# Kernel tuning notes

Measured on AMD Instinct MI355X. Metric: run time of the kernel, lower is better.

The kernel has to match this reference:

```python
import jax, jax.numpy as jnp
import numpy as np

L = 2048
E = 1024
H = 16
D = E // H


def setup_inputs() -> dict:
    key = jax.random.key(0)
    ks = jax.random.split(key, 9)
    inp = {
        "values": jax.random.normal(ks[0], (L, E), dtype=jnp.float32),
        "keys": jax.random.normal(ks[1], (L, E), dtype=jnp.float32),
        "query": jax.random.normal(ks[2], (L, E), dtype=jnp.float32),
        "dist_matrix": jax.random.uniform(ks[3], (L, L), dtype=jnp.float32),
        "Wv": jax.random.normal(ks[4], (E, E), dtype=jnp.float32) * 0.02,
        "Wk": jax.random.normal(ks[5], (E, E), dtype=jnp.float32) * 0.02,
        "Wq": jax.random.normal(ks[6], (E, E), dtype=jnp.float32) * 0.02,
        "Wo": jax.random.normal(ks[7], (E, E), dtype=jnp.float32) * 0.02,
        "bo": jax.random.normal(ks[8], (E,), dtype=jnp.float32) * 0.02,
    }
    return inp


def reference(values, keys, query, dist_matrix, Wv, Wk, Wq, Wo, bo):
    # Linear projections (torch Linear: x @ W.T), then split heads: [L, H, D]
    v = (values @ Wv.T).reshape(L, H, D)
    k = (keys @ Wk.T).reshape(L, H, D)
    q = (query @ Wq.T).reshape(L, H, D)

    # energy: [H, Lq, Lk]
    energy = jnp.einsum("qhd,khd->hqk", q, k)

    # distance bias: zeros -> inf, then 1/(d+1); broadcast over heads
    dm = jnp.where(dist_matrix == 0, jnp.inf, dist_matrix)
    bias = 1.0 / (dm + 1.0)
    energy = energy + bias[None, :, :]

    attn = jax.nn.softmax(energy / jnp.sqrt(jnp.float32(E)), axis=2)

    out = jnp.einsum("hql,lhd->qhd", attn, v).reshape(L, H * D)
    return out @ Wo.T + bo
```

## Files before the change

### kernel.cpp

```cpp
#include <hip/hip_runtime.h>


#define L_SEQ 2048
#define E_DIM 1024
#define H_HEADS 16
#define D_HEAD 64
#define KSPLIT 4
#define OSPLIT 2

typedef unsigned short u16;
typedef unsigned int u32;
typedef __attribute__((ext_vector_type(8))) short bf16x8;
typedef __attribute__((ext_vector_type(8))) unsigned short u16x8;
typedef __attribute__((ext_vector_type(4))) unsigned short u16x4;
typedef __attribute__((ext_vector_type(4))) float f32x4;

#define C_LOG2E_32 0.045084220027780106f

__device__ __forceinline__ float bf2f(u16 u) {
  union { u32 i; float f; } v; v.i = ((u32)u) << 16; return v.f;
}
__device__ __forceinline__ u16 f2bf(float f) {
  union { float f; u32 i; } v; v.f = f;
  u32 u = v.i;
  u += 0x7FFFu + ((u >> 16) & 1u);
  return (u16)(u >> 16);
}
__device__ __forceinline__ u32 pack_bf16_pair(float lo, float hi) {
  union { float f; u32 u; } a, b;
  a.f = lo; b.f = hi;
  return __builtin_amdgcn_perm(b.u + 0x8000u, a.u + 0x8000u, 0x07060302u);
}
__device__ __forceinline__ void gload16(const u16* g, u16* l) {
  __builtin_amdgcn_global_load_lds(
      (const __attribute__((address_space(1))) u32*)g,
      (__attribute__((address_space(3))) u32*)l, 16, 0, 0);
}

__global__ void cvt_all(const float* __restrict__ xq, const float* __restrict__ xk,
                        const float* __restrict__ xv,
                        const float* __restrict__ wq, const float* __restrict__ wk,
                        const float* __restrict__ wv, const float* __restrict__ wo,
                        const float* __restrict__ dist, const float* __restrict__ bo,
                        u16* oq, u16* ok, u16* ov,
                        u16* owq, u16* owk, u16* owv, u16* owo, u16* obias,
                        float* __restrict__ outp)
{
  size_t gid = (size_t)blockIdx.x * 256 + threadIdx.x;
  const size_t NQ = 524288;
  const size_t NW = 262144;
  const size_t DL = 1048576;
  const size_t FILL = 3 * NQ + 4 * NW + DL;

  if (gid >= FILL) {
    size_t off = (gid - FILL) * 4;
    int n = (int)(off & (E_DIM - 1));
    *(f32x4*)&outp[off] = *(const f32x4*)&bo[n];
    return;
  }

  const float* src; u16* dst; size_t off; bool isb = false;
  if      (gid <     NQ)           { src = xq;   dst = oq;    off = gid; }
  else if (gid < 2 * NQ)           { src = xk;   dst = ok;    off = gid - NQ; }
  else if (gid < 3 * NQ)           { src = xv;   dst = ov;    off = gid - 2 * NQ; }
  else if (gid < 3 * NQ + NW)      { src = wq;   dst = owq;   off = gid - 3 * NQ; }
  else if (gid < 3 * NQ + 2 * NW)  { src = wk;   dst = owk;   off = gid - 3 * NQ - NW; }
  else if (gid < 3 * NQ + 3 * NW)  { src = wv;   dst = owv;   off = gid - 3 * NQ - 2 * NW; }
  else if (gid < 3 * NQ + 4 * NW)  { src = wo;   dst = owo;   off = gid - 3 * NQ - 3 * NW; }
  else { src = dist; dst = obias; off = gid - 3 * NQ - 4 * NW; isb = true; }

  f32x4 v = *(const f32x4*)&src[off * 4];
  u16x4 o;
#pragma unroll
  for (int j = 0; j < 4; ++j) {
    float f = v[j];
    if (isb) f = (f == 0.f) ? 0.f : C_LOG2E_32 / (f + 1.f);
    o[j] = f2bf(f);
  }
  *(u16x4*)&dst[off * 4] = o;
}

#define TM 64
#define TN 128
#define BK 32

template<int OUTMODE>
__global__ __launch_bounds__(256, 4) void gemm_pd(
    const u16* __restrict__ A0, const u16* __restrict__ B0, void* __restrict__ C0,
    const u16* __restrict__ A1, const u16* __restrict__ B1, void* __restrict__ C1,
    const u16* __restrict__ A2, const u16* __restrict__ B2, void* __restrict__ C2,
    int M, int N, int K)
{
  const u16* A; const u16* B; void* C;
  if (OUTMODE == 2)         { A = A0; B = B0; C = C0; }
  else if (blockIdx.z == 0) { A = A0; B = B0; C = C0; }
  else if (blockIdx.z == 1) { A = A1; B = B1; C = C1; }
  else                      { A = A2; B = B2; C = C2; }

  __shared__ __align__(16) u16 As[2][TM * BK];
  __shared__ __align__(16) u16 Bs[2][TN * BK];

  const int m0 = blockIdx.y * TM;
  const int n0 = blockIdx.x * TN;
  const int t = threadIdx.x;
  const int wave = t >> 6;
  const int lane = t & 63;
  const int quad = lane >> 4;
  const int col  = lane & 15;
  const int wm = (wave >> 1) * 32;
  const int wn = (wave & 1) * 64;

  const int sr = lane >> 2;
  const int sg = ((lane & 3) ^ ((lane >> 3) & 3)) * 8;
  const u16* gA  = A + (size_t)(m0 + wave * 16 + sr) * K + sg;
  const u16* gB0 = B + (size_t)(n0 + wave * 16 + sr) * K + sg;
  const u16* gB1 = B + (size_t)(n0 + 64 + wave * 16 + sr) * K + sg;
  const int lA  = (wave * 16) * BK;
  const int lB0 = (wave * 16) * BK;
  const int lB1 = (64 + wave * 16) * BK;

  const int kbeg = (OUTMODE == 2) ? blockIdx.z * (K / OSPLIT) : 0;
  const int kend = (OUTMODE == 2) ? kbeg + K / OSPLIT : K;

  f32x4 acc[2][4];
#pragma unroll
  for (int i = 0; i < 2; ++i)
#pragma unroll
    for (int j = 0; j < 4; ++j) acc[i][j] = (f32x4){0.f, 0.f, 0.f, 0.f};

  gload16(gA + kbeg, &As[0][lA]);
  gload16(gB0 + kbeg, &Bs[0][lB0]);
  gload16(gB1 + kbeg, &Bs[0][lB1]);

  const int slot8 = (quad ^ ((col >> 1) & 3)) * 8;

  int buf = 0;
  for (int k0 = kbeg; k0 < kend; k0 += BK) {
    __syncthreads();
    int nk = k0 + BK;
    if (nk < kend) {
      gload16(gA + nk, &As[buf ^ 1][lA]);
      gload16(gB0 + nk, &Bs[buf ^ 1][lB0]);
      gload16(gB1 + nk, &Bs[buf ^ 1][lB1]);
    }

    bf16x8 af[2], bfr[4];
#pragma unroll
    for (int i = 0; i < 2; ++i)
      af[i] = *(const bf16x8*)&As[buf][(wm + i * 16 + col) * BK + slot8];
#pragma unroll
    for (int j = 0; j < 4; ++j)
      bfr[j] = *(const bf16x8*)&Bs[buf][(wn + j * 16 + col) * BK + slot8];

#pragma unroll
    for (int i = 0; i < 2; ++i)
#pragma unroll
      for (int j = 0; j < 4; ++j)
        acc[i][j] = __builtin_amdgcn_mfma_f32_16x16x32_bf16(af[i], bfr[j], acc[i][j], 0, 0, 0);

    buf ^= 1;
  }

  const bool transC = (OUTMODE == 0) && (blockIdx.z == 2);
#pragma unroll
  for (int i = 0; i < 2; ++i) {
    int rowb = m0 + wm + i * 16 + quad * 4;
#pragma unroll
    for (int j = 0; j < 4; ++j) {
      int cn = n0 + wn + j * 16 + col;
      if (OUTMODE == 2) {
#pragma unroll
        for (int r = 0; r < 4; ++r)
          unsafeAtomicAdd(&((float*)C)[(size_t)(rowb + r) * N + cn], acc[i][j][r]);
      } else if (transC) {
        u16x4 pk;
#pragma unroll
        for (int r = 0; r < 4; ++r) pk[r] = f2bf(acc[i][j][r]);
        *(u16x4*)&((u16*)C)[(size_t)cn * M + rowb] = pk;
      } else {
#pragma unroll
        for (int r = 0; r < 4; ++r)
          ((u16*)C)[(size_t)(rowb + r) * N + cn] = f2bf(acc[i][j][r]);
      }
    }
  }
}

#define FK 32
#define PLDV 40

__global__ __launch_bounds__(256, 7) void flash5(
    const u16* __restrict__ Q, const u16* __restrict__ Kp,
    const u16* __restrict__ Vt, const u16* __restrict__ Bb,
    u16* __restrict__ Op, float* __restrict__ lp)
{
  __shared__ __align__(16) u16 Ks[2][FK * 64];
  __shared__ __align__(16) u16 Vs[2][D_HEAD * FK];
  __shared__ __align__(16) u16 Ps[4][16][PLDV];

  const int h  = blockIdx.y;
  const int q0 = blockIdx.x * 64;
  const int z  = blockIdx.z;
  const int hoff = h * D_HEAD;
  const int kbase = z * (L_SEQ / KSPLIT);
  const int NT = (L_SEQ / KSPLIT) / FK;
  const int t = threadIdx.x;
  const int wave = t >> 6;
  const int lane = t & 63;
  const int quad = lane >> 4;
  const int col  = lane & 15;

  bf16x8 qf[2];
  {
    const u16* qrow = Q + (size_t)(q0 + wave * 16 + col) * E_DIM + hoff;
    qf[0] = *(const bf16x8*)(qrow + quad * 8);
    qf[1] = *(const bf16x8*)(qrow + 32 + quad * 8);
  }

  const int krow = wave * 8 + (lane >> 3);
  const int kg = ((lane & 7) ^ (lane >> 3)) * 8;
  const u16* gK = Kp + (size_t)krow * E_DIM + hoff + kg;
  u16* lK = &Ks[0][wave * 8 * 64];

  const int vrow = wave * 16 + (lane >> 2);
  const int vg = ((lane & 3) ^ ((lane >> 4) & 3)) * 8;
  const u16* gV = Vt + (size_t)(hoff + vrow) * L_SEQ + vg;
  u16* lV = &Vs[0][wave * 16 * FK];

  float l_lane = 0.f;
  f32x4 oacc[4];
#pragma unroll
  for (int td = 0; td < 4; ++td) oacc[td] = (f32x4){0.f, 0.f, 0.f, 0.f};

  const u16* brow = Bb + (size_t)(q0 + wave * 16 + col) * L_SEQ;

  gload16(gK + (size_t)kbase * E_DIM, lK);
  gload16(gV + kbase, lV);
  u16x4 bv[2], bn[2] = {(u16x4){0,0,0,0}, (u16x4){0,0,0,0}};
  bv[0] = *(const u16x4*)&brow[kbase + quad * 4];
  bv[1] = *(const u16x4*)&brow[kbase + 16 + quad * 4];

  const int ks0 = (quad ^ (col & 7)) * 8;
  const int ks1 = ((quad + 4) ^ (col & 7)) * 8;
  const int vsl = (quad ^ ((col >> 2) & 3)) * 8;

  int buf = 0;
  for (int kt = 0; kt < NT; ++kt) {
    const int k0 = kbase + kt * FK;
    __syncthreads();
    if (kt + 1 < NT) {
      const int nk = k0 + FK;
      gload16(gK + (size_t)nk * E_DIM, lK + (buf ^ 1 ? 0 : 0) + (buf ^ 1) * (FK * 64) - buf * 0);
      gload16(gV + nk, lV + (buf ^ 1) * (D_HEAD * FK));
      bn[0] = *(const u16x4*)&brow[nk + quad * 4];
      bn[1] = *(const u16x4*)&brow[nk + 16 + quad * 4];
    }
    const u16* Kb = &Ks[buf][0];
    const u16* Vb = &Vs[buf][0];

#pragma unroll
    for (int tt = 0; tt < 2; ++tt) {
      const u16* kr = &Kb[(tt * 16 + col) * 64];
      f32x4 a = (f32x4){0.f, 0.f, 0.f, 0.f};
      a = __builtin_amdgcn_mfma_f32_16x16x32_bf16(*(const bf16x8*)&kr[ks0], qf[0], a, 0, 0, 0);
      a = __builtin_amdgcn_mfma_f32_16x16x32_bf16(*(const bf16x8*)&kr[ks1], qf[1], a, 0, 0, 0);
      float p[4];
#pragma unroll
      for (int r = 0; r < 4; ++r) {
        p[r] = __builtin_amdgcn_exp2f(fmaf(a[r], C_LOG2E_32, bf2f(bv[tt][r])));
        l_lane += p[r];
      }
      uint2 w;
      w.x = pack_bf16_pair(p[0], p[1]);
      w.y = pack_bf16_pair(p[2], p[3]);
      *(uint2*)&Ps[wave][col][tt * 16 + quad * 4] = w;
    }

    {
      bf16x8 pf = *(const bf16x8*)&Ps[wave][col][quad * 8];
#pragma unroll
      for (int td = 0; td < 4; ++td) {
        bf16x8 vf = *(const bf16x8*)&Vb[(td * 16 + col) * FK + vsl];
        oacc[td] = __builtin_amdgcn_mfma_f32_16x16x32_bf16(pf, vf, oacc[td], 0, 0, 0);
      }
    }

    bv[0] = bn[0]; bv[1] = bn[1];
    buf ^= 1;
  }

  l_lane += __shfl_xor(l_lane, 16);
  l_lane += __shfl_xor(l_lane, 32);
  if (lane < 16)
    lp[((size_t)z * L_SEQ + q0 + wave * 16 + lane) * H_HEADS + h] = l_lane;

  const int qrow_mine = q0 + wave * 16 + quad * 4;
#pragma unroll
  for (int td = 0; td < 4; ++td)
#pragma unroll
    for (int r = 0; r < 4; ++r)
      Op[((size_t)z * L_SEQ + qrow_mine + r) * E_DIM + hoff + td * 16 + col] = f2bf(oacc[td][r]);
}

__global__ void merge_attn(const u16* __restrict__ Op, const float* __restrict__ lp,
                           u16* __restrict__ AOb)
{
  size_t gid = (size_t)blockIdx.x * 256 + threadIdx.x;
  size_t idx = gid * 4;
  int q = (int)(idx >> 10);
  int e = (int)(idx & 1023);
  int h = e >> 6;
  float o[4] = {0.f, 0.f, 0.f, 0.f};
  float lsum = 0.f;
#pragma unroll
  for (int s = 0; s < KSPLIT; ++s) {
    u16x4 pv = *(const u16x4*)&Op[((size_t)s * L_SEQ + q) * E_DIM + e];
#pragma unroll
    for (int j = 0; j < 4; ++j) o[j] += bf2f(pv[j]);
    lsum += lp[((size_t)s * L_SEQ + q) * H_HEADS + h];
  }
  float inv = 1.f / lsum;
  u16x4 pk;
#pragma unroll
  for (int j = 0; j < 4; ++j) pk[j] = f2bf(o[j] * inv);
  *(u16x4*)&AOb[idx] = pk;
}

extern "C" void kernel_launch(void* const* d_in, const int* in_sizes, int n_in,
                              void* d_out, int out_size, void* d_ws, size_t ws_size,
                              hipStream_t stream)
{
  const float* values = (const float*)d_in[0];
  const float* keys   = (const float*)d_in[1];
  const float* query  = (const float*)d_in[2];
  const float* dist   = (const float*)d_in[3];
  const float* Wv     = (const float*)d_in[4];
  const float* Wk     = (const float*)d_in[5];
  const float* Wq     = (const float*)d_in[6];
  const float* Wo     = (const float*)d_in[7];
  const float* bo     = (const float*)d_in[8];
  float* out = (float*)d_out;

  const size_t MB = (size_t)1 << 20;
  char* w = (char*)d_ws;
  u16* xq  = (u16*)(w + 0 * MB);
  u16* xk  = (u16*)(w + 4 * MB);
  u16* xv  = (u16*)(w + 8 * MB);
  u16* wqb = (u16*)(w + 12 * MB);
  u16* wkb = (u16*)(w + 14 * MB);
  u16* wvb = (u16*)(w + 16 * MB);
  u16* wob = (u16*)(w + 18 * MB);
  u16* Bb  = (u16*)(w + 20 * MB);
  u16* Qh  = (u16*)(w + 28 * MB);
  u16* Kh  = (u16*)(w + 32 * MB);
  u16* Vth = (u16*)(w + 36 * MB);
  u16* AOb = (u16*)(w + 40 * MB);
  float* lp = (float*)(w + 44 * MB);
  u16* Op  = (u16*)(w + 0 * MB);

  cvt_all<<<16384, 256, 0, stream>>>(query, keys, values, Wq, Wk, Wv, Wo, dist, bo,
                                     xq, xk, xv, wqb, wkb, wvb, wob, Bb, out);

  dim3 gProj(E_DIM / TN, L_SEQ / TM, 3);
  gemm_pd<0><<<gProj, 256, 0, stream>>>(xq, wqb, Qh,
                                        xk, wkb, Kh,
                                        xv, wvb, Vth,
                                        L_SEQ, E_DIM, E_DIM);

  dim3 gAttn(L_SEQ / 64, H_HEADS, KSPLIT);
  flash5<<<gAttn, 256, 0, stream>>>(Qh, Kh, Vth, Bb, Op, lp);

  merge_attn<<<(L_SEQ * E_DIM / 4) / 256, 256, 0, stream>>>(Op, lp, AOb);

  dim3 gOut(E_DIM / TN, L_SEQ / TM, OSPLIT);
  gemm_pd<2><<<gOut, 256, 0, stream>>>(AOb, wob, out,
                                       AOb, wob, out,
                                       AOb, wob, out,
                                       L_SEQ, E_DIM, E_DIM);
}
```

Measured before the change: 217.4 us.

## Enlarge GEMM and attention tiles for operand reuse; widen conversion kernel

```diff
diff --git a/kernel.cpp b/kernel.cpp
--- a/kernel.cpp
+++ b/kernel.cpp
@@ -47,15 +47,16 @@
                         float* __restrict__ outp)
 {
   size_t gid = (size_t)blockIdx.x * 256 + threadIdx.x;
-  const size_t NQ = 524288;
-  const size_t NW = 262144;
-  const size_t DL = 1048576;
+  const size_t NQ = 262144;
+  const size_t NW = 131072;
+  const size_t DL = 524288;
   const size_t FILL = 3 * NQ + 4 * NW + DL;
 
   if (gid >= FILL) {
-    size_t off = (gid - FILL) * 4;
+    size_t off = (gid - FILL) * 8;
     int n = (int)(off & (E_DIM - 1));
     *(f32x4*)&outp[off] = *(const f32x4*)&bo[n];
+    *(f32x4*)&outp[off + 4] = *(const f32x4*)&bo[n + 4];
     return;
   }
 
@@ -69,23 +70,27 @@
   else if (gid < 3 * NQ + 4 * NW)  { src = wo;   dst = owo;   off = gid - 3 * NQ - 3 * NW; }
   else { src = dist; dst = obias; off = gid - 3 * NQ - 4 * NW; isb = true; }
 
-  f32x4 v = *(const f32x4*)&src[off * 4];
-  u16x4 o;
+  f32x4 v0 = *(const f32x4*)&src[off * 8];
+  f32x4 v1 = *(const f32x4*)&src[off * 8 + 4];
+  u16x8 o;
 #pragma unroll
   for (int j = 0; j < 4; ++j) {
-    float f = v[j];
-    if (isb) f = (f == 0.f) ? 0.f : C_LOG2E_32 / (f + 1.f);
-    o[j] = f2bf(f);
-  }
-  *(u16x4*)&dst[off * 4] = o;
-}
-
-#define TM 64
+    float f0 = v0[j], f1 = v1[j];
+    if (isb) {
+      f0 = (f0 == 0.f) ? 0.f : C_LOG2E_32 / (f0 + 1.f);
+      f1 = (f1 == 0.f) ? 0.f : C_LOG2E_32 / (f1 + 1.f);
+    }
+    o[j] = f2bf(f0); o[j + 4] = f2bf(f1);
+  }
+  *(u16x8*)&dst[off * 8] = o;
+}
+
+#define TM 128
 #define TN 128
 #define BK 32
 
 template<int OUTMODE>
-__global__ __launch_bounds__(256, 4) void gemm_pd(
+__global__ __launch_bounds__(256, 3) void gemm_pd(
     const u16* __restrict__ A0, const u16* __restrict__ B0, void* __restrict__ C0,
     const u16* __restrict__ A1, const u16* __restrict__ B1, void* __restrict__ C1,
     const u16* __restrict__ A2, const u16* __restrict__ B2, void* __restrict__ C2,
@@ -107,30 +112,29 @@
   const int lane = t & 63;
   const int quad = lane >> 4;
   const int col  = lane & 15;
-  const int wm = (wave >> 1) * 32;
+  const int wm = (wave >> 1) * 64;
   const int wn = (wave & 1) * 64;
 
   const int sr = lane >> 2;
   const int sg = ((lane & 3) ^ ((lane >> 3) & 3)) * 8;
-  const u16* gA  = A + (size_t)(m0 + wave * 16 + sr) * K + sg;
-  const u16* gB0 = B + (size_t)(n0 + wave * 16 + sr) * K + sg;
-  const u16* gB1 = B + (size_t)(n0 + 64 + wave * 16 + sr) * K + sg;
-  const int lA  = (wave * 16) * BK;
-  const int lB0 = (wave * 16) * BK;
-  const int lB1 = (64 + wave * 16) * BK;
+  const u16* gA = A + (size_t)(m0 + wave * 32 + sr) * K + sg;
+  const u16* gB = B + (size_t)(n0 + wave * 32 + sr) * K + sg;
+  const int lo0 = (wave * 32) * BK;
+  const int lo1 = (wave * 32 + 16) * BK;
 
   const int kbeg = (OUTMODE == 2) ? blockIdx.z * (K / OSPLIT) : 0;
   const int kend = (OUTMODE == 2) ? kbeg + K / OSPLIT : K;
 
-  f32x4 acc[2][4];
-#pragma unroll
-  for (int i = 0; i < 2; ++i)
+  f32x4 acc[4][4];
+#pragma unroll
+  for (int i = 0; i < 4; ++i)
 #pragma unroll
     for (int j = 0; j < 4; ++j) acc[i][j] = (f32x4){0.f, 0.f, 0.f, 0.f};
 
-  gload16(gA + kbeg, &As[0][lA]);
-  gload16(gB0 + kbeg, &Bs[0][lB0]);
-  gload16(gB1 + kbeg, &Bs[0][lB1]);
+  gload16(gA + kbeg, &As[0][lo0]);
+  gload16(gA + (size_t)16 * K + kbeg, &As[0][lo1]);
+  gload16(gB + kbeg, &Bs[0][lo0]);
+  gload16(gB + (size_t)16 * K + kbeg, &Bs[0][lo1]);
 
   const int slot8 = (quad ^ ((col >> 1) & 3)) * 8;
 
@@ -139,21 +143,22 @@
     __syncthreads();
     int nk = k0 + BK;
     if (nk < kend) {
-      gload16(gA + nk, &As[buf ^ 1][lA]);
-      gload16(gB0 + nk, &Bs[buf ^ 1][lB0]);
-      gload16(gB1 + nk, &Bs[buf ^ 1][lB1]);
-    }
-
-    bf16x8 af[2], bfr[4];
-#pragma unroll
-    for (int i = 0; i < 2; ++i)
+      gload16(gA + nk, &As[buf ^ 1][lo0]);
+      gload16(gA + (size_t)16 * K + nk, &As[buf ^ 1][lo1]);
+      gload16(gB + nk, &Bs[buf ^ 1][lo0]);
+      gload16(gB + (size_t)16 * K + nk, &Bs[buf ^ 1][lo1]);
+    }
+
+    bf16x8 af[4], bfr[4];
+#pragma unroll
+    for (int i = 0; i < 4; ++i)
       af[i] = *(const bf16x8*)&As[buf][(wm + i * 16 + col) * BK + slot8];
 #pragma unroll
     for (int j = 0; j < 4; ++j)
       bfr[j] = *(const bf16x8*)&Bs[buf][(wn + j * 16 + col) * BK + slot8];
 
 #pragma unroll
-    for (int i = 0; i < 2; ++i)
+    for (int i = 0; i < 4; ++i)
 #pragma unroll
       for (int j = 0; j < 4; ++j)
         acc[i][j] = __builtin_amdgcn_mfma_f32_16x16x32_bf16(af[i], bfr[j], acc[i][j], 0, 0, 0);
@@ -163,7 +168,7 @@
 
   const bool transC = (OUTMODE == 0) && (blockIdx.z == 2);
 #pragma unroll
-  for (int i = 0; i < 2; ++i) {
+  for (int i = 0; i < 4; ++i) {
     int rowb = m0 + wm + i * 16 + quad * 4;
 #pragma unroll
     for (int j = 0; j < 4; ++j) {
@@ -189,17 +194,17 @@
 #define FK 32
 #define PLDV 40
 
-__global__ __launch_bounds__(256, 7) void flash5(
+__global__ __launch_bounds__(256, 4) void flash6(
     const u16* __restrict__ Q, const u16* __restrict__ Kp,
     const u16* __restrict__ Vt, const u16* __restrict__ Bb,
     u16* __restrict__ Op, float* __restrict__ lp)
 {
   __shared__ __align__(16) u16 Ks[2][FK * 64];
   __shared__ __align__(16) u16 Vs[2][D_HEAD * FK];
-  __shared__ __align__(16) u16 Ps[4][16][PLDV];
+  __shared__ __align__(16) u16 Ps[4][2][16][PLDV];
 
   const int h  = blockIdx.y;
-  const int q0 = blockIdx.x * 64;
+  const int q0 = blockIdx.x * 128;
   const int z  = blockIdx.z;
   const int hoff = h * D_HEAD;
   const int kbase = z * (L_SEQ / KSPLIT);
@@ -210,35 +215,39 @@
   const int quad = lane >> 4;
   const int col  = lane & 15;
 
-  bf16x8 qf[2];
-  {
-    const u16* qrow = Q + (size_t)(q0 + wave * 16 + col) * E_DIM + hoff;
-    qf[0] = *(const bf16x8*)(qrow + quad * 8);
-    qf[1] = *(const bf16x8*)(qrow + 32 + quad * 8);
+  bf16x8 qf[2][2];
+  const u16* brow[2];
+#pragma unroll
+  for (int s = 0; s < 2; ++s) {
+    const int qs = q0 + wave * 32 + s * 16;
+    const u16* qrow = Q + (size_t)(qs + col) * E_DIM + hoff;
+    qf[s][0] = *(const bf16x8*)(qrow + quad * 8);
+    qf[s][1] = *(const bf16x8*)(qrow + 32 + quad * 8);
+    brow[s] = Bb + (size_t)(qs + col) * L_SEQ;
   }
 
   const int krow = wave * 8 + (lane >> 3);
   const int kg = ((lane & 7) ^ (lane >> 3)) * 8;
   const u16* gK = Kp + (size_t)krow * E_DIM + hoff + kg;
-  u16* lK = &Ks[0][wave * 8 * 64];
-
   const int vrow = wave * 16 + (lane >> 2);
   const int vg = ((lane & 3) ^ ((lane >> 4) & 3)) * 8;
   const u16* gV = Vt + (size_t)(hoff + vrow) * L_SEQ + vg;
-  u16* lV = &Vs[0][wave * 16 * FK];
-
-  float l_lane = 0.f;
-  f32x4 oacc[4];
-#pragma unroll
-  for (int td = 0; td < 4; ++td) oacc[td] = (f32x4){0.f, 0.f, 0.f, 0.f};
-
-  const u16* brow = Bb + (size_t)(q0 + wave * 16 + col) * L_SEQ;
-
-  gload16(gK + (size_t)kbase * E_DIM, lK);
-  gload16(gV + kbase, lV);
-  u16x4 bv[2], bn[2] = {(u16x4){0,0,0,0}, (u16x4){0,0,0,0}};
-  bv[0] = *(const u16x4*)&brow[kbase + quad * 4];
-  bv[1] = *(const u16x4*)&brow[kbase + 16 + quad * 4];
+
+  float l_lane[2] = {0.f, 0.f};
+  f32x4 oacc[2][4];
+#pragma unroll
+  for (int s = 0; s < 2; ++s)
+#pragma unroll
+    for (int td = 0; td < 4; ++td) oacc[s][td] = (f32x4){0.f, 0.f, 0.f, 0.f};
+
+  gload16(gK + (size_t)kbase * E_DIM, &Ks[0][wave * 8 * 64]);
+  gload16(gV + kbase, &Vs[0][wave * 16 * FK]);
+  u16x4 bv[2][2], bn[2][2];
+#pragma unroll
+  for (int s = 0; s < 2; ++s) {
+    bv[s][0] = *(const u16x4*)&brow[s][kbase + quad * 4];
+    bv[s][1] = *(const u16x4*)&brow[s][kbase + 16 + quad * 4];
+  }
 
   const int ks0 = (quad ^ (col & 7)) * 8;
   const int ks1 = ((quad + 4) ^ (col & 7)) * 8;
@@ -250,10 +259,13 @@
     __syncthreads();
     if (kt + 1 < NT) {
       const int nk = k0 + FK;
-      gload16(gK + (size_t)nk * E_DIM, lK + (buf ^ 1 ? 0 : 0) + (buf ^ 1) * (FK * 64) - buf * 0);
-      gload16(gV + nk, lV + (buf ^ 1) * (D_HEAD * FK));
-      bn[0] = *(const u16x4*)&brow[nk + quad * 4];
-      bn[1] = *(const u16x4*)&brow[nk + 16 + quad * 4];
+      gload16(gK + (size_t)nk * E_DIM, &Ks[buf ^ 1][wave * 8 * 64]);
+      gload16(gV + nk, &Vs[buf ^ 1][wave * 16 * FK]);
+#pragma unroll
+      for (int s = 0; s < 2; ++s) {
+        bn[s][0] = *(const u16x4*)&brow[s][nk + quad * 4];
+        bn[s][1] = *(const u16x4*)&brow[s][nk + 16 + quad * 4];
+      }
     }
     const u16* Kb = &Ks[buf][0];
     const u16* Vb = &Vs[buf][0];
@@ -261,45 +273,58 @@
 #pragma unroll
     for (int tt = 0; tt < 2; ++tt) {
       const u16* kr = &Kb[(tt * 16 + col) * 64];
-      f32x4 a = (f32x4){0.f, 0.f, 0.f, 0.f};
-      a = __builtin_amdgcn_mfma_f32_16x16x32_bf16(*(const bf16x8*)&kr[ks0], qf[0], a, 0, 0, 0);
-      a = __builtin_amdgcn_mfma_f32_16x16x32_bf16(*(const bf16x8*)&kr[ks1], qf[1], a, 0, 0, 0);
-      float p[4];
-#pragma unroll
-      for (int r = 0; r < 4; ++r) {
-        p[r] = __builtin_amdgcn_exp2f(fmaf(a[r], C_LOG2E_32, bf2f(bv[tt][r])));
-        l_lane += p[r];
+      bf16x8 kf0 = *(const bf16x8*)&kr[ks0];
+      bf16x8 kf1 = *(const bf16x8*)&kr[ks1];
+#pragma unroll
+      for (int s = 0; s < 2; ++s) {
+        f32x4 a = (f32x4){0.f, 0.f, 0.f, 0.f};
+        a = __builtin_amdgcn_mfma_f32_16x16x32_bf16(kf0, qf[s][0], a, 0, 0, 0);
+        a = __builtin_amdgcn_mfma_f32_16x16x32_bf16(kf1, qf[s][1], a, 0, 0, 0);
+        float p[4];
+#pragma unroll
+        for (int r = 0; r < 4; ++r) {
+          p[r] = __builtin_amdgcn_exp2f(fmaf(a[r], C_LOG2E_32, bf2f(bv[s][tt][r])));
+          l_lane[s] += p[r];
+        }
+        uint2 w;
+        w.x = pack_bf16_pair(p[0], p[1]);
+        w.y = pack_bf16_pair(p[2], p[3]);
+        *(uint2*)&Ps[wave][s][col][tt * 16 + quad * 4] = w;
       }
-      uint2 w;
-      w.x = pack_bf16_pair(p[0], p[1]);
-      w.y = pack_bf16_pair(p[2], p[3]);
-      *(uint2*)&Ps[wave][col][tt * 16 + quad * 4] = w;
-    }
-
-    {
-      bf16x8 pf = *(const bf16x8*)&Ps[wave][col][quad * 8];
+    }
+
+#pragma unroll
+    for (int s = 0; s < 2; ++s) {
+      bf16x8 pf = *(const bf16x8*)&Ps[wave][s][col][quad * 8];
 #pragma unroll
       for (int td = 0; td < 4; ++td) {
         bf16x8 vf = *(const bf16x8*)&Vb[(td * 16 + col) * FK + vsl];
-        oacc[td] = __builtin_amdgcn_mfma_f32_16x16x32_bf16(pf, vf, oacc[td], 0, 0, 0);
+        oacc[s][td] = __builtin_amdgcn_mfma_f32_16x16x32_bf16(pf, vf, oacc[s][td], 0, 0, 0);
       }
     }
 
-    bv[0] = bn[0]; bv[1] = bn[1];
+#pragma unroll
+    for (int s = 0; s < 2; ++s) { bv[s][0] = bn[s][0]; bv[s][1] = bn[s][1]; }
     buf ^= 1;
   }
 
-  l_lane += __shfl_xor(l_lane, 16);
-  l_lane += __shfl_xor(l_lane, 32);
-  if (lane < 16)
-    lp[((size_t)z * L_SEQ + q0 + wave * 16 + lane) * H_HEADS + h] = l_lane;
-
-  const int qrow_mine = q0 + wave * 16 + quad * 4;
-#pragma unroll
-  for (int td = 0; td < 4; ++td)
-#pragma unroll
-    for (int r = 0; r < 4; ++r)
-      Op[((size_t)z * L_SEQ + qrow_mine + r) * E_DIM + hoff + td * 16 + col] = f2bf(oacc[td][r]);
+#pragma unroll
+  for (int s = 0; s < 2; ++s) {
+    l_lane[s] += __shfl_xor(l_lane[s], 16);
+    l_lane[s] += __shfl_xor(l_lane[s], 32);
+    if (lane < 16)
+      lp[((size_t)z * L_SEQ + q0 + wave * 32 + s * 16 + lane) * H_HEADS + h] = l_lane[s];
+  }
+
+#pragma unroll
+  for (int s = 0; s < 2; ++s) {
+    const int qrow_mine = q0 + wave * 32 + s * 16 + quad * 4;
+#pragma unroll
+    for (int td = 0; td < 4; ++td)
+#pragma unroll
+      for (int r = 0; r < 4; ++r)
+        Op[((size_t)z * L_SEQ + qrow_mine + r) * E_DIM + hoff + td * 16 + col] = f2bf(oacc[s][td][r]);
+  }
 }
 
 __global__ void merge_attn(const u16* __restrict__ Op, const float* __restrict__ lp,
@@ -358,8 +383,8 @@
   float* lp = (float*)(w + 44 * MB);
   u16* Op  = (u16*)(w + 0 * MB);
 
-  cvt_all<<<16384, 256, 0, stream>>>(query, keys, values, Wq, Wk, Wv, Wo, dist, bo,
-                                     xq, xk, xv, wqb, wkb, wvb, wob, Bb, out);
+  cvt_all<<<8192, 256, 0, stream>>>(query, keys, values, Wq, Wk, Wv, Wo, dist, bo,
+                                    xq, xk, xv, wqb, wkb, wvb, wob, Bb, out);
 
   dim3 gProj(E_DIM / TN, L_SEQ / TM, 3);
   gemm_pd<0><<<gProj, 256, 0, stream>>>(xq, wqb, Qh,
@@ -367,8 +392,8 @@
                                         xv, wvb, Vth,
                                         L_SEQ, E_DIM, E_DIM);
 
-  dim3 gAttn(L_SEQ / 64, H_HEADS, KSPLIT);
-  flash5<<<gAttn, 256, 0, stream>>>(Qh, Kh, Vth, Bb, Op, lp);
+  dim3 gAttn(L_SEQ / 128, H_HEADS, KSPLIT);
+  flash6<<<gAttn, 256, 0, stream>>>(Qh, Kh, Vth, Bb, Op, lp);
 
   merge_attn<<<(L_SEQ * E_DIM / 4) / 256, 256, 0, stream>>>(Op, lp, AOb);
 
```

Result: faster. 207.2 us (-4.7%).
